# Kernel optimization log

Hardware: AMD Instinct MI355X
Metric: run time of the kernel (lower is better)

## Reference

```python
import jax, jax.numpy as jnp
import numpy as np

B, H, W, C = 16, 128, 128, 64
PH, PW = 2, 2  # pool_size == strides, 'valid' padding


def setup_inputs() -> dict:
    key = jax.random.key(0)
    k0, k1, k2, k3 = jax.random.split(key, 4)
    shp = (B, H, W, C)
    return {
        "x0": jax.random.normal(k0, shp, dtype=jnp.float32),
        "x1": jax.random.normal(k1, shp, dtype=jnp.float32),
        "x2": jax.random.normal(k2, shp, dtype=jnp.float32),
        "x3": jax.random.normal(k3, shp, dtype=jnp.float32),
    }


def _windows(t, ph, pw):
    # (B,H,W,C,...) -> (B, H//ph, W//pw, C, ph*pw, ...) with row-major window
    # flattening (h then w), matching tf.nn.max_pool_with_argmax index order.
    b, h, w, c = t.shape[:4]
    rest = t.shape[4:]
    t = t.reshape((b, h // ph, ph, w // pw, pw, c) + rest)
    perm = (0, 1, 3, 5, 2, 4) + tuple(range(6, 6 + len(rest)))
    t = t.transpose(perm)
    return t.reshape((b, h // ph, w // pw, c, ph * pw) + rest)


def reference(x0, x1, x2, x3):
    # Stack quaternion components: (B,H,W,C,4)
    x = jnp.stack([x0, x1, x2, x3], axis=-1)
    # Euclidean norm over the 4 components: (B,H,W,C)
    norm = jnp.sqrt(jnp.sum(x * x, axis=-1))
    # Non-overlapping 2x2 windows (pool_size == strides, VALID padding)
    norm_w = _windows(norm, PH, PW)           # (B,Ho,Wo,C,4win)
    idx = jnp.argmax(norm_w, axis=-1)         # first-max tie-break, like TF
    x_w = _windows(x, PH, PW)                 # (B,Ho,Wo,C,4win,4comp)
    pooled = jnp.take_along_axis(x_w, idx[..., None, None], axis=4)
    pooled = pooled.squeeze(4)                # (B,Ho,Wo,C,4comp)
    return (pooled[..., 0], pooled[..., 1], pooled[..., 2], pooled[..., 3])


if __name__ == "__main__":
    out = reference(**setup_inputs())
    print([o.shape for o in out])
```

## Files before the change

### kernel.cpp

```cpp
#include <hip/hip_runtime.h>

#define BN 16
#define HN 128
#define WN 128
#define CN 64
#define HO (HN / 2)
#define WO (WN / 2)
#define C4 (CN / 4)
#define OUT_PER (BN * HO * WO * CN)
#define ROW4 (WN * C4)

__device__ __forceinline__ float4 qnorm4(const float4 a, const float4 b,
                                         const float4 c, const float4 d) {
#pragma clang fp contract(off)
    float4 r;
    r.x = sqrtf(((a.x * a.x + b.x * b.x) + c.x * c.x) + d.x * d.x);
    r.y = sqrtf(((a.y * a.y + b.y * b.y) + c.y * c.y) + d.y * d.y);
    r.z = sqrtf(((a.z * a.z + b.z * b.z) + c.z * c.z) + d.z * d.z);
    r.w = sqrtf(((a.w * a.w + b.w * b.w) + c.w * c.w) + d.w * d.w);
    return r;
}

#define UPD_ELEM(f)                                                            \
    do {                                                                       \
        bool m = n.f > bn.f;                                                   \
        bn.f = m ? n.f : bn.f;                                                 \
        v0.f = m ? a0.f : v0.f;                                                \
        v1.f = m ? a1.f : v1.f;                                                \
        v2.f = m ? a2.f : v2.f;                                                \
        v3.f = m ? a3.f : v3.f;                                                \
    } while (0)

__global__ __launch_bounds__(256) void maxnorm_pool_kernel(
    const float4* __restrict__ x0, const float4* __restrict__ x1,
    const float4* __restrict__ x2, const float4* __restrict__ x3,
    float4* __restrict__ out) {
    const int t = blockIdx.x * 256 + threadIdx.x;
    const int c4  = t & (C4 - 1);
    const int pix = t >> 4;
    const int wo  = pix & (WO - 1);
    const int rst = pix >> 6;
    const int ho  = rst & (HO - 1);
    const int b   = rst >> 6;

    const int base = ((b * HN + 2 * ho) * WN + 2 * wo) * C4 + c4;
    const int o01 = base + C4;
    const int o10 = base + ROW4;
    const int o11 = base + ROW4 + C4;

    float4 w0a = x0[base], w0b = x1[base], w0c = x2[base], w0d = x3[base];
    float4 w1a = x0[o01],  w1b = x1[o01],  w1c = x2[o01],  w1d = x3[o01];
    float4 w2a = x0[o10],  w2b = x1[o10],  w2c = x2[o10],  w2d = x3[o10];
    float4 w3a = x0[o11],  w3b = x1[o11],  w3c = x2[o11],  w3d = x3[o11];

    float4 bn = qnorm4(w0a, w0b, w0c, w0d);
    float4 v0 = w0a, v1 = w0b, v2 = w0c, v3 = w0d;

    {
        float4 a0 = w1a, a1 = w1b, a2 = w1c, a3 = w1d;
        float4 n = qnorm4(a0, a1, a2, a3);
        UPD_ELEM(x); UPD_ELEM(y); UPD_ELEM(z); UPD_ELEM(w);
    }
    {
        float4 a0 = w2a, a1 = w2b, a2 = w2c, a3 = w2d;
        float4 n = qnorm4(a0, a1, a2, a3);
        UPD_ELEM(x); UPD_ELEM(y); UPD_ELEM(z); UPD_ELEM(w);
    }
    {
        float4 a0 = w3a, a1 = w3b, a2 = w3c, a3 = w3d;
        float4 n = qnorm4(a0, a1, a2, a3);
        UPD_ELEM(x); UPD_ELEM(y); UPD_ELEM(z); UPD_ELEM(w);
    }

    const int oi = pix * C4 + c4;
    out[oi]                  = v0;
    out[OUT_PER / 4 + oi]    = v1;
    out[2 * (OUT_PER / 4) + oi] = v2;
    out[3 * (OUT_PER / 4) + oi] = v3;
}

extern "C" void kernel_launch(void* const* d_in, const int* in_sizes, int n_in,
                              void* d_out, int out_size, void* d_ws, size_t ws_size,
                              hipStream_t stream) {
    const float4* x0 = (const float4*)d_in[0];
    const float4* x1 = (const float4*)d_in[1];
    const float4* x2 = (const float4*)d_in[2];
    const float4* x3 = (const float4*)d_in[3];
    float4* out = (float4*)d_out;

    const int total_threads = BN * HO * WO * C4;
    const int block = 256;
    const int grid = total_threads / block;
    maxnorm_pool_kernel<<<grid, block, 0, stream>>>(x0, x1, x2, x3, out);
}
```

Baseline: 259.2 us.

## Split 2x2 window across lane pairs with shuffle-based horizontal reduction

Each thread now loads one float4 column position from two input rows, so a wavefront reads contiguous row data instead of each thread gathering a whole 2x2 window. The horizontal half of the window is resolved by exchanging the vertical winner with the partner lane via xor-16 shuffles, with tie-break logic that keeps first-max ordering. This doubles the thread count, and half the lanes sit idle during the stores. It also adds shuffle traffic in exchange for more coalesced loads. The kernel is memory-bound, so the gain depends on whether the old access pattern was already being served well by the cache.

```diff
diff --git a/kernel.cpp b/kernel.cpp
--- a/kernel.cpp
+++ b/kernel.cpp
@@ -4,11 +4,11 @@
 #define HN 128
 #define WN 128
 #define CN 64
-#define HO (HN / 2)
-#define WO (WN / 2)
-#define C4 (CN / 4)
-#define OUT_PER (BN * HO * WO * CN)
+#define HO 64
+#define WO 64
+#define C4 16
 #define ROW4 (WN * C4)
+#define OUTQ (BN * HO * WO * C4)
 
 __device__ __forceinline__ float4 qnorm4(const float4 a, const float4 b,
                                          const float4 c, const float4 d) {
@@ -21,14 +21,35 @@
     return r;
 }
 
-#define UPD_ELEM(f)                                                            \
+__device__ __forceinline__ float4 shfl16(float4 v) {
+    float4 r;
+    r.x = __shfl_xor(v.x, 16);
+    r.y = __shfl_xor(v.y, 16);
+    r.z = __shfl_xor(v.z, 16);
+    r.w = __shfl_xor(v.w, 16);
+    return r;
+}
+
+#define VERT(f, k)                                                             \
     do {                                                                       \
-        bool m = n.f > bn.f;                                                   \
-        bn.f = m ? n.f : bn.f;                                                 \
-        v0.f = m ? a0.f : v0.f;                                                \
-        v1.f = m ? a1.f : v1.f;                                                \
-        v2.f = m ? a2.f : v2.f;                                                \
-        v3.f = m ? a3.f : v3.f;                                                \
+        bool m = n1.f > n0.f;                                                  \
+        bn.f = m ? n1.f : n0.f;                                                \
+        s0.f = m ? a0r1.f : a0r0.f;                                            \
+        s1.f = m ? a1r1.f : a1r0.f;                                            \
+        s2.f = m ? a2r1.f : a2r0.f;                                            \
+        s3.f = m ? a3r1.f : a3r0.f;                                            \
+        rows |= (m ? (1 << (k)) : 0);                                          \
+    } while (0)
+
+#define HORZ(f, k)                                                             \
+    do {                                                                       \
+        bool rE = (rows >> (k)) & 1;                                           \
+        bool rO = (rowsO >> (k)) & 1;                                          \
+        bool tO = (bnO.f > bn.f) || ((bnO.f == bn.f) && rE && !rO);            \
+        s0.f = tO ? p0.f : s0.f;                                               \
+        s1.f = tO ? p1.f : s1.f;                                               \
+        s2.f = tO ? p2.f : s2.f;                                               \
+        s3.f = tO ? p3.f : s3.f;                                               \
     } while (0)
 
 __global__ __launch_bounds__(256) void maxnorm_pool_kernel(
@@ -36,47 +57,39 @@
     const float4* __restrict__ x2, const float4* __restrict__ x3,
     float4* __restrict__ out) {
     const int t = blockIdx.x * 256 + threadIdx.x;
-    const int c4  = t & (C4 - 1);
-    const int pix = t >> 4;
-    const int wo  = pix & (WO - 1);
-    const int rst = pix >> 6;
-    const int ho  = rst & (HO - 1);
-    const int b   = rst >> 6;
+    const int within = t & (ROW4 - 1);
+    const int rowIdx = t >> 11;
+    const int ho = rowIdx & (HO - 1);
+    const int b  = rowIdx >> 6;
 
-    const int base = ((b * HN + 2 * ho) * WN + 2 * wo) * C4 + c4;
-    const int o01 = base + C4;
-    const int o10 = base + ROW4;
-    const int o11 = base + ROW4 + C4;
+    const int g0 = (b * HN + 2 * ho) * ROW4 + within;
+    const int g1 = g0 + ROW4;
 
-    float4 w0a = x0[base], w0b = x1[base], w0c = x2[base], w0d = x3[base];
-    float4 w1a = x0[o01],  w1b = x1[o01],  w1c = x2[o01],  w1d = x3[o01];
-    float4 w2a = x0[o10],  w2b = x1[o10],  w2c = x2[o10],  w2d = x3[o10];
-    float4 w3a = x0[o11],  w3b = x1[o11],  w3c = x2[o11],  w3d = x3[o11];
+    float4 a0r0 = x0[g0], a1r0 = x1[g0], a2r0 = x2[g0], a3r0 = x3[g0];
+    float4 a0r1 = x0[g1], a1r1 = x1[g1], a2r1 = x2[g1], a3r1 = x3[g1];
 
-    float4 bn = qnorm4(w0a, w0b, w0c, w0d);
-    float4 v0 = w0a, v1 = w0b, v2 = w0c, v3 = w0d;
+    float4 n0 = qnorm4(a0r0, a1r0, a2r0, a3r0);
+    float4 n1 = qnorm4(a0r1, a1r1, a2r1, a3r1);
 
-    {
-        float4 a0 = w1a, a1 = w1b, a2 = w1c, a3 = w1d;
-        float4 n = qnorm4(a0, a1, a2, a3);
-        UPD_ELEM(x); UPD_ELEM(y); UPD_ELEM(z); UPD_ELEM(w);
+    float4 bn, s0, s1, s2, s3;
+    int rows = 0;
+    VERT(x, 0); VERT(y, 1); VERT(z, 2); VERT(w, 3);
+
+    float4 bnO = shfl16(bn);
+    float4 p0 = shfl16(s0), p1 = shfl16(s1), p2 = shfl16(s2), p3 = shfl16(s3);
+    int rowsO = __shfl_xor(rows, 16);
+
+    HORZ(x, 0); HORZ(y, 1); HORZ(z, 2); HORZ(w, 3);
+
+    if (((threadIdx.x >> 4) & 1) == 0) {
+        const int c4 = within & (C4 - 1);
+        const int wo = within >> 5;
+        const int oi = ((b * HO + ho) * WO + wo) * C4 + c4;
+        out[oi]            = s0;
+        out[OUTQ + oi]     = s1;
+        out[2 * OUTQ + oi] = s2;
+        out[3 * OUTQ + oi] = s3;
     }
-    {
-        float4 a0 = w2a, a1 = w2b, a2 = w2c, a3 = w2d;
-        float4 n = qnorm4(a0, a1, a2, a3);
-        UPD_ELEM(x); UPD_ELEM(y); UPD_ELEM(z); UPD_ELEM(w);
-    }
-    {
-        float4 a0 = w3a, a1 = w3b, a2 = w3c, a3 = w3d;
-        float4 n = qnorm4(a0, a1, a2, a3);
-        UPD_ELEM(x); UPD_ELEM(y); UPD_ELEM(z); UPD_ELEM(w);
-    }
-
-    const int oi = pix * C4 + c4;
-    out[oi]                  = v0;
-    out[OUT_PER / 4 + oi]    = v1;
-    out[2 * (OUT_PER / 4) + oi] = v2;
-    out[3 * (OUT_PER / 4) + oi] = v3;
 }
 
 extern "C" void kernel_launch(void* const* d_in, const int* in_sizes, int n_in,
@@ -88,7 +101,7 @@
     const float4* x3 = (const float4*)d_in[3];
     float4* out = (float4*)d_out;
 
-    const int total_threads = BN * HO * WO * C4;
+    const int total_threads = BN * HO * ROW4;
     const int block = 256;
     const int grid = total_threads / block;
     maxnorm_pool_kernel<<<grid, block, 0, stream>>>(x0, x1, x2, x3, out);
```

Measured after the change: 255.9 us. About the same (-1.2%).
